# Performance work log

Hardware: AMD Instinct MI355X
Metric: run time of the kernel (lower is better)

The kernel has to match this reference:

```python
import jax, jax.numpy as jnp
import numpy as np

DIM = 1024
NUM_HEADS = 16
NUM_KV_HEADS = 4
HEAD_DIM = 64
SOFT_CAP = 50.0
EPS = 1e-6


def setup_inputs() -> dict:
    key = jax.random.key(0)
    ks = jax.random.split(key, 8)
    B, T, S = 4, 128, 256
    q_dim = NUM_HEADS * HEAD_DIM
    kv_dim = NUM_KV_HEADS * HEAD_DIM
    s = 0.02
    return {
        "agent_tokens": jax.random.normal(ks[0], (B, T, DIM), jnp.float32),
        "z_tokens": jax.random.normal(ks[1], (B, T, S, DIM), jnp.float32),
        "Wq": jax.random.normal(ks[2], (DIM, q_dim), jnp.float32) * s,
        "Wk": jax.random.normal(ks[3], (DIM, kv_dim), jnp.float32) * s,
        "Wv": jax.random.normal(ks[4], (DIM, kv_dim), jnp.float32) * s,
        "Wo": jax.random.normal(ks[5], (q_dim, DIM), jnp.float32) * s,
        "q_gamma": 1.0 + jax.random.normal(ks[6], (HEAD_DIM,), jnp.float32) * s,
        "k_gamma": 1.0 + jax.random.normal(ks[7], (HEAD_DIM,), jnp.float32) * s,
    }


def _rmsnorm(x, gamma):
    # normalize over head_dim (last axis)
    var = jnp.mean(jnp.square(x), axis=-1, keepdims=True)
    return x * jax.lax.rsqrt(var + EPS) * gamma


def reference(agent_tokens, z_tokens, Wq, Wk, Wv, Wo, q_gamma, k_gamma):
    B, T, D = agent_tokens.shape
    S = z_tokens.shape[2]
    H, Hkv, hd = NUM_HEADS, NUM_KV_HEADS, HEAD_DIM
    G = H // Hkv
    scale = hd ** -0.5

    q = (agent_tokens @ Wq).reshape(B, T, H, hd)          # (B,T,H,hd)  single query per frame
    k = (z_tokens @ Wk).reshape(B, T, S, Hkv, hd)          # (B,T,S,Hkv,hd)
    v = (z_tokens @ Wv).reshape(B, T, S, Hkv, hd)

    q = _rmsnorm(q, q_gamma)
    k = _rmsnorm(k, k_gamma)

    # GQA: view q as (B,T,Hkv,G,hd) so each KV head serves G query heads
    qg = q.reshape(B, T, Hkv, G, hd)
    scores = jnp.einsum('btkgd,btskd->btkgs', qg, k) * scale   # (B,T,Hkv,G,S)
    scores = SOFT_CAP * jnp.tanh(scores / SOFT_CAP)
    attn = jax.nn.softmax(scores, axis=-1)
    out = jnp.einsum('btkgs,btskd->btkgd', attn, v)            # (B,T,Hkv,G,hd)
    out = out.reshape(B, T, H * hd)
    return out @ Wo                                            # (B,T,D)
```

## Files before the change

kernel.cpp:

```cpp
#include <hip/hip_runtime.h>
#include <hip/hip_bf16.h>

#define SOFTCAP_ 50.0f
#define EPS_ 1e-6f

typedef __attribute__((ext_vector_type(8))) short bf16x8;
typedef __attribute__((ext_vector_type(4))) float f32x4;

__device__ __forceinline__ unsigned short f2bf(float f) {
    unsigned u = __float_as_uint(f);
    u += 0x7FFFu + ((u >> 16) & 1u);
    return (unsigned short)(u >> 16);
}

__global__ void wkv_swizzle(const float* __restrict__ Wk, const float* __restrict__ Wv,
                            unsigned short* __restrict__ wkv) {
    int tid = blockIdx.x * 256 + threadIdx.x;
    int l = tid & 63;
    int nb = (tid >> 6) & 31;
    int kb = tid >> 11;
    int n = nb * 16 + (l & 15);
    int kbase = kb * 32 + ((l >> 4) << 3);
    const float* src = (n < 256) ? (Wk + n) : (Wv + (n - 256));
    unsigned short r[8];
#pragma unroll
    for (int j = 0; j < 8; ++j) r[j] = f2bf(src[(size_t)(kbase + j) * 256]);
    uint4 o;
    o.x = (unsigned)r[0] | ((unsigned)r[1] << 16);
    o.y = (unsigned)r[2] | ((unsigned)r[3] << 16);
    o.z = (unsigned)r[4] | ((unsigned)r[5] << 16);
    o.w = (unsigned)r[6] | ((unsigned)r[7] << 16);
    *(uint4*)(wkv + (size_t)tid * 8) = o;
}

__global__ __launch_bounds__(256) void qproj_kernel(
    const float* __restrict__ agent, const float* __restrict__ Wq,
    const float* __restrict__ q_gamma, float* __restrict__ ws_q)
{
    __shared__ float srows[8][1024];
    int cg = blockIdx.x, rg = blockIdx.y;
    int t = threadIdx.x;
#pragma unroll
    for (int j = 0; j < 8; ++j) {
        int f = j * 256 + t;
        int row = f >> 8, c4 = f & 255;
        *(float4*)&srows[row][c4 * 4] =
            *(const float4*)(agent + (size_t)(rg * 8 + row) * 1024 + c4 * 4);
    }
    __syncthreads();
    int c = cg * 64 + (t & 63);
    int rq = t >> 6;
    float acc0 = 0.f, acc1 = 0.f;
    for (int k = 0; k < 1024; k += 4) {
        float w0 = Wq[(size_t)(k + 0) * 1024 + c];
        float w1 = Wq[(size_t)(k + 1) * 1024 + c];
        float w2 = Wq[(size_t)(k + 2) * 1024 + c];
        float w3 = Wq[(size_t)(k + 3) * 1024 + c];
        float4 a0 = *(const float4*)&srows[rq * 2][k];
        float4 a1 = *(const float4*)&srows[rq * 2 + 1][k];
        acc0 += a0.x * w0 + a0.y * w1 + a0.z * w2 + a0.w * w3;
        acc1 += a1.x * w0 + a1.y * w1 + a1.z * w2 + a1.w * w3;
    }
    float g = q_gamma[t & 63];
    float ss0 = acc0 * acc0, ss1 = acc1 * acc1;
#pragma unroll
    for (int d = 1; d < 64; d <<= 1) { ss0 += __shfl_xor(ss0, d); ss1 += __shfl_xor(ss1, d); }
    float rs0 = rsqrtf(ss0 * (1.0f / 64.0f) + EPS_);
    float rs1 = rsqrtf(ss1 * (1.0f / 64.0f) + EPS_);
    ws_q[(size_t)(rg * 8 + rq * 2 + 0) * 1024 + c] = acc0 * rs0 * g;
    ws_q[(size_t)(rg * 8 + rq * 2 + 1) * 1024 + c] = acc1 * rs1 * g;
}

__global__ __launch_bounds__(256, 3) void kv_attn_kernel(
    const float* __restrict__ z, const unsigned short* __restrict__ wkv,
    const float* __restrict__ ws_q, const float* __restrict__ k_gamma,
    float* __restrict__ ws_att)
{
    __shared__ __align__(16) unsigned short zlds[32 * 256];
    const int bt = blockIdx.x;
    const int tid = threadIdx.x;
    const int head = tid >> 6;
    const int l = tid & 63, l15 = l & 15, lg = l >> 4;

    float qn[4][4], kgm[4];
#pragma unroll
    for (int g = 0; g < 4; ++g)
#pragma unroll
        for (int ni = 0; ni < 4; ++ni)
            qn[g][ni] = ws_q[(size_t)bt * 1024 + (head * 4 + g) * 64 + ni * 16 + l15];
#pragma unroll
    for (int ni = 0; ni < 4; ++ni) kgm[ni] = k_gamma[ni * 16 + l15];

    float out_acc[4][4] = {};
    float denom[4] = {};

    for (int sc = 0; sc < 8; ++sc) {
        f32x4 acc[2][8];
#pragma unroll
        for (int mi = 0; mi < 2; ++mi)
#pragma unroll
            for (int ni = 0; ni < 8; ++ni) acc[mi][ni] = (f32x4){0.f, 0.f, 0.f, 0.f};

        for (int sl = 0; sl < 4; ++sl) {
            __syncthreads();
#pragma unroll
            for (int jb = 0; jb < 2; ++jb) {
                float4 v[4];
#pragma unroll
                for (int i = 0; i < 4; ++i) {
                    int f = (jb * 4 + i) * 256 + tid;
                    int row = f >> 6, c4 = f & 63;
                    v[i] = *(const float4*)(z + (size_t)(bt * 256 + sc * 32 + row) * 1024
                                              + sl * 256 + c4 * 4);
                }
#pragma unroll
                for (int i = 0; i < 4; ++i) {
                    int f = (jb * 4 + i) * 256 + tid;
                    int row = f >> 6, c4 = f & 63;
                    unsigned lo = (unsigned)f2bf(v[i].x) | ((unsigned)f2bf(v[i].y) << 16);
                    unsigned hi = (unsigned)f2bf(v[i].z) | ((unsigned)f2bf(v[i].w) << 16);
                    int byteoff = ((row * 512) + c4 * 8) ^ ((row & 7) << 4);
                    *(uint2*)((char*)zlds + byteoff) = (uint2){lo, hi};
                }
            }
            __syncthreads();
#pragma unroll
            for (int ksl = 0; ksl < 8; ++ksl) {
                const int kb = sl * 8 + ksl;
                int boff0 = ((l15 * 512) + ksl * 64 + lg * 16) ^ ((l15 & 7) << 4);
                bf16x8 a0 = *(const bf16x8*)((const char*)zlds + boff0);
                bf16x8 a1 = *(const bf16x8*)((const char*)zlds + boff0 + 8192);
                bf16x8 b[8];
#pragma unroll
                for (int ni = 0; ni < 8; ++ni) {
                    int nb = (ni < 4) ? (head * 4 + ni) : (16 + head * 4 + ni - 4);
                    b[ni] = *(const bf16x8*)(wkv + ((size_t)(kb * 32 + nb) * 64 + l) * 8);
                }
#pragma unroll
                for (int ni = 0; ni < 8; ++ni) {
                    acc[0][ni] = __builtin_amdgcn_mfma_f32_16x16x32_bf16(a0, b[ni], acc[0][ni], 0, 0, 0);
                    acc[1][ni] = __builtin_amdgcn_mfma_f32_16x16x32_bf16(a1, b[ni], acc[1][ni], 0, 0, 0);
                }
            }
        }
#pragma unroll
        for (int mi = 0; mi < 2; ++mi) {
#pragma unroll
            for (int r = 0; r < 4; ++r) {
                float k0 = acc[mi][0][r], k1 = acc[mi][1][r], k2 = acc[mi][2][r], k3 = acc[mi][3][r];
                float ss = k0 * k0 + k1 * k1 + k2 * k2 + k3 * k3;
                ss += __shfl_xor(ss, 1); ss += __shfl_xor(ss, 2);
                ss += __shfl_xor(ss, 4); ss += __shfl_xor(ss, 8);
                float rs = rsqrtf(ss * (1.0f / 64.0f) + EPS_);
                k0 *= rs * kgm[0]; k1 *= rs * kgm[1]; k2 *= rs * kgm[2]; k3 *= rs * kgm[3];
#pragma unroll
                for (int g = 0; g < 4; ++g) {
                    float sp = qn[g][0] * k0 + qn[g][1] * k1 + qn[g][2] * k2 + qn[g][3] * k3;
                    sp += __shfl_xor(sp, 1); sp += __shfl_xor(sp, 2);
                    sp += __shfl_xor(sp, 4); sp += __shfl_xor(sp, 8);
                    float scv = sp * 0.125f;
                    float e2 = __expf(scv * (2.0f / SOFTCAP_));
                    float th = 1.0f - 2.0f / (e2 + 1.0f);
                    float p = __expf(SOFTCAP_ * th);
                    denom[g] += p;
                    out_acc[g][0] += p * acc[mi][4][r];
                    out_acc[g][1] += p * acc[mi][5][r];
                    out_acc[g][2] += p * acc[mi][6][r];
                    out_acc[g][3] += p * acc[mi][7][r];
                }
            }
        }
    }
#pragma unroll
    for (int g = 0; g < 4; ++g) {
        float d = denom[g];
        d += __shfl_xor(d, 16); d += __shfl_xor(d, 32);
        float inv = 1.0f / d;
#pragma unroll
        for (int ni = 0; ni < 4; ++ni) {
            float o = out_acc[g][ni];
            o += __shfl_xor(o, 16); o += __shfl_xor(o, 32);
            if (lg == 0)
                ws_att[(size_t)bt * 1024 + (head * 4 + g) * 64 + ni * 16 + l15] = o * inv;
        }
    }
}

__global__ __launch_bounds__(256) void oproj_kernel(
    const float* __restrict__ att, const float* __restrict__ Wo,
    float* __restrict__ out)
{
    __shared__ float srows[8][1024];
    int cg = blockIdx.x, rg = blockIdx.y;
    int t = threadIdx.x;
#pragma unroll
    for (int j = 0; j < 8; ++j) {
        int f = j * 256 + t;
        int row = f >> 8, c4 = f & 255;
        *(float4*)&srows[row][c4 * 4] =
            *(const float4*)(att + (size_t)(rg * 8 + row) * 1024 + c4 * 4);
    }
    __syncthreads();
    int c = cg * 64 + (t & 63);
    int rq = t >> 6;
    float acc0 = 0.f, acc1 = 0.f;
    for (int k = 0; k < 1024; k += 4) {
        float w0 = Wo[(size_t)(k + 0) * 1024 + c];
        float w1 = Wo[(size_t)(k + 1) * 1024 + c];
        float w2 = Wo[(size_t)(k + 2) * 1024 + c];
        float w3 = Wo[(size_t)(k + 3) * 1024 + c];
        float4 a0 = *(const float4*)&srows[rq * 2][k];
        float4 a1 = *(const float4*)&srows[rq * 2 + 1][k];
        acc0 += a0.x * w0 + a0.y * w1 + a0.z * w2 + a0.w * w3;
        acc1 += a1.x * w0 + a1.y * w1 + a1.z * w2 + a1.w * w3;
    }
    out[(size_t)(rg * 8 + rq * 2 + 0) * 1024 + c] = acc0;
    out[(size_t)(rg * 8 + rq * 2 + 1) * 1024 + c] = acc1;
}

extern "C" void kernel_launch(void* const* d_in, const int* in_sizes, int n_in,
                              void* d_out, int out_size, void* d_ws, size_t ws_size,
                              hipStream_t stream) {
    const float* agent = (const float*)d_in[0];
    const float* z     = (const float*)d_in[1];
    const float* Wq    = (const float*)d_in[2];
    const float* Wk    = (const float*)d_in[3];
    const float* Wv    = (const float*)d_in[4];
    const float* Wo    = (const float*)d_in[5];
    const float* qg    = (const float*)d_in[6];
    const float* kg    = (const float*)d_in[7];
    float* out = (float*)d_out;

    char* ws = (char*)d_ws;
    float* ws_q   = (float*)ws;
    float* ws_att = (float*)(ws + (2u << 20));
    unsigned short* ws_wkv = (unsigned short*)(ws + (4u << 20));

    hipLaunchKernelGGL(wkv_swizzle, dim3(256), dim3(256), 0, stream, Wk, Wv, ws_wkv);
    hipLaunchKernelGGL(qproj_kernel, dim3(16, 64), dim3(256), 0, stream, agent, Wq, qg, ws_q);
    hipLaunchKernelGGL(kv_attn_kernel, dim3(512), dim3(256), 0, stream, z, ws_wkv, ws_q, kg, ws_att);
    hipLaunchKernelGGL(oproj_kernel, dim3(16, 64), dim3(256), 0, stream, ws_att, Wo, out);
}
```

Measured before the change: 400.6 us.

## Split KV-attention over four S-chunks per frame with atomic partial accumulation

The attention kernel now launches four blocks per (b,t) frame, each covering 64 of the 256 z rows, instead of one block per frame. Partial numerators and softmax denominators are combined with atomicAdd into zeroed workspace, and normalization moves into the output-projection load. The aim is more parallelism: 2048 blocks instead of 512 to fill the GPU's compute units and hide memory latency. The cost is two memsets plus atomics. Partial exp sums are added without a running max, which relies on the soft cap bounding the scores. The query load is moved inside the chunk loop to reduce register pressure.

After: 541.1 us. 1.35x slower.

```diff
diff --git a/kernel.cpp b/kernel.cpp
--- a/kernel.cpp
+++ b/kernel.cpp
@@ -74,27 +74,23 @@
 __global__ __launch_bounds__(256, 3) void kv_attn_kernel(
     const float* __restrict__ z, const unsigned short* __restrict__ wkv,
     const float* __restrict__ ws_q, const float* __restrict__ k_gamma,
-    float* __restrict__ ws_att)
+    float* __restrict__ att_raw, float* __restrict__ den)
 {
     __shared__ __align__(16) unsigned short zlds[32 * 256];
-    const int bt = blockIdx.x;
+    const int blk = blockIdx.x;
+    const int bt = blk >> 2, q = blk & 3;
     const int tid = threadIdx.x;
     const int head = tid >> 6;
     const int l = tid & 63, l15 = l & 15, lg = l >> 4;
 
-    float qn[4][4], kgm[4];
-#pragma unroll
-    for (int g = 0; g < 4; ++g)
-#pragma unroll
-        for (int ni = 0; ni < 4; ++ni)
-            qn[g][ni] = ws_q[(size_t)bt * 1024 + (head * 4 + g) * 64 + ni * 16 + l15];
+    float kgm[4];
 #pragma unroll
     for (int ni = 0; ni < 4; ++ni) kgm[ni] = k_gamma[ni * 16 + l15];
 
     float out_acc[4][4] = {};
     float denom[4] = {};
 
-    for (int sc = 0; sc < 8; ++sc) {
+    for (int sc = 0; sc < 2; ++sc) {
         f32x4 acc[2][8];
 #pragma unroll
         for (int mi = 0; mi < 2; ++mi)
@@ -110,7 +106,7 @@
                 for (int i = 0; i < 4; ++i) {
                     int f = (jb * 4 + i) * 256 + tid;
                     int row = f >> 6, c4 = f & 63;
-                    v[i] = *(const float4*)(z + (size_t)(bt * 256 + sc * 32 + row) * 1024
+                    v[i] = *(const float4*)(z + (size_t)(bt * 256 + q * 64 + sc * 32 + row) * 1024
                                               + sl * 256 + c4 * 4);
                 }
 #pragma unroll
@@ -130,19 +126,32 @@
                 int boff0 = ((l15 * 512) + ksl * 64 + lg * 16) ^ ((l15 & 7) << 4);
                 bf16x8 a0 = *(const bf16x8*)((const char*)zlds + boff0);
                 bf16x8 a1 = *(const bf16x8*)((const char*)zlds + boff0 + 8192);
-                bf16x8 b[8];
-#pragma unroll
-                for (int ni = 0; ni < 8; ++ni) {
-                    int nb = (ni < 4) ? (head * 4 + ni) : (16 + head * 4 + ni - 4);
-                    b[ni] = *(const bf16x8*)(wkv + ((size_t)(kb * 32 + nb) * 64 + l) * 8);
-                }
-#pragma unroll
-                for (int ni = 0; ni < 8; ++ni) {
-                    acc[0][ni] = __builtin_amdgcn_mfma_f32_16x16x32_bf16(a0, b[ni], acc[0][ni], 0, 0, 0);
-                    acc[1][ni] = __builtin_amdgcn_mfma_f32_16x16x32_bf16(a1, b[ni], acc[1][ni], 0, 0, 0);
+                bf16x8 bk[4];
+#pragma unroll
+                for (int ni = 0; ni < 4; ++ni)
+                    bk[ni] = *(const bf16x8*)(wkv + ((size_t)(kb * 32 + head * 4 + ni) * 64 + l) * 8);
+#pragma unroll
+                for (int ni = 0; ni < 4; ++ni) {
+                    acc[0][ni] = __builtin_amdgcn_mfma_f32_16x16x32_bf16(a0, bk[ni], acc[0][ni], 0, 0, 0);
+                    acc[1][ni] = __builtin_amdgcn_mfma_f32_16x16x32_bf16(a1, bk[ni], acc[1][ni], 0, 0, 0);
+                }
+                bf16x8 bv[4];
+#pragma unroll
+                for (int ni = 0; ni < 4; ++ni)
+                    bv[ni] = *(const bf16x8*)(wkv + ((size_t)(kb * 32 + 16 + head * 4 + ni) * 64 + l) * 8);
+#pragma unroll
+                for (int ni = 0; ni < 4; ++ni) {
+                    acc[0][4 + ni] = __builtin_amdgcn_mfma_f32_16x16x32_bf16(a0, bv[ni], acc[0][4 + ni], 0, 0, 0);
+                    acc[1][4 + ni] = __builtin_amdgcn_mfma_f32_16x16x32_bf16(a1, bv[ni], acc[1][4 + ni], 0, 0, 0);
                 }
             }
         }
+        float qn[4][4];
+#pragma unroll
+        for (int g = 0; g < 4; ++g)
+#pragma unroll
+            for (int ni = 0; ni < 4; ++ni)
+                qn[g][ni] = ws_q[(size_t)bt * 1024 + (head * 4 + g) * 64 + ni * 16 + l15];
 #pragma unroll
         for (int mi = 0; mi < 2; ++mi) {
 #pragma unroll
@@ -175,20 +184,20 @@
     for (int g = 0; g < 4; ++g) {
         float d = denom[g];
         d += __shfl_xor(d, 16); d += __shfl_xor(d, 32);
-        float inv = 1.0f / d;
+        if (l == 0) atomicAdd(den + bt * 16 + head * 4 + g, d);
 #pragma unroll
         for (int ni = 0; ni < 4; ++ni) {
             float o = out_acc[g][ni];
             o += __shfl_xor(o, 16); o += __shfl_xor(o, 32);
             if (lg == 0)
-                ws_att[(size_t)bt * 1024 + (head * 4 + g) * 64 + ni * 16 + l15] = o * inv;
+                atomicAdd(att_raw + (size_t)bt * 1024 + (head * 4 + g) * 64 + ni * 16 + l15, o);
         }
     }
 }
 
 __global__ __launch_bounds__(256) void oproj_kernel(
-    const float* __restrict__ att, const float* __restrict__ Wo,
-    float* __restrict__ out)
+    const float* __restrict__ att_raw, const float* __restrict__ den,
+    const float* __restrict__ Wo, float* __restrict__ out)
 {
     __shared__ float srows[8][1024];
     int cg = blockIdx.x, rg = blockIdx.y;
@@ -197,8 +206,11 @@
     for (int j = 0; j < 8; ++j) {
         int f = j * 256 + t;
         int row = f >> 8, c4 = f & 255;
-        *(float4*)&srows[row][c4 * 4] =
-            *(const float4*)(att + (size_t)(rg * 8 + row) * 1024 + c4 * 4);
+        float4 v = *(const float4*)(att_raw + (size_t)(rg * 8 + row) * 1024 + c4 * 4);
+        float dv = den[(rg * 8 + row) * 16 + (c4 >> 4)];
+        float inv = 1.0f / dv;
+        v.x *= inv; v.y *= inv; v.z *= inv; v.w *= inv;
+        *(float4*)&srows[row][c4 * 4] = v;
     }
     __syncthreads();
     int c = cg * 64 + (t & 63);
@@ -232,12 +244,15 @@
     float* out = (float*)d_out;
 
     char* ws = (char*)d_ws;
-    float* ws_q   = (float*)ws;
-    float* ws_att = (float*)(ws + (2u << 20));
+    float* ws_q    = (float*)ws;
+    float* att_raw = (float*)(ws + (2u << 20));
     unsigned short* ws_wkv = (unsigned short*)(ws + (4u << 20));
-
+    float* den     = (float*)(ws + (5u << 20));
+
+    hipMemsetAsync(att_raw, 0, 2u << 20, stream);
+    hipMemsetAsync(den, 0, 512 * 16 * sizeof(float), stream);
     hipLaunchKernelGGL(wkv_swizzle, dim3(256), dim3(256), 0, stream, Wk, Wv, ws_wkv);
     hipLaunchKernelGGL(qproj_kernel, dim3(16, 64), dim3(256), 0, stream, agent, Wq, qg, ws_q);
-    hipLaunchKernelGGL(kv_attn_kernel, dim3(512), dim3(256), 0, stream, z, ws_wkv, ws_q, kg, ws_att);
-    hipLaunchKernelGGL(oproj_kernel, dim3(16, 64), dim3(256), 0, stream, ws_att, Wo, out);
-}
+    hipLaunchKernelGGL(kv_attn_kernel, dim3(2048), dim3(256), 0, stream, z, ws_wkv, ws_q, kg, att_raw, den);
+    hipLaunchKernelGGL(oproj_kernel, dim3(16, 64), dim3(256), 0, stream, att_raw, den, Wo, out);
+}
```
